# Optimization experiments

Hardware: AMD Instinct MI355X
Metric: run time of the kernel (lower is better)

Reference implementation:

```python
import jax, jax.numpy as jnp
import numpy as np

B, F = 1048576, 128


def setup_inputs() -> dict:
    key = jax.random.key(0)
    ks = jax.random.split(key, 16)
    def w(k, shape):
        return jax.random.normal(k, shape, dtype=jnp.float32) * 0.1
    x = jax.random.uniform(ks[0], (B, F), dtype=jnp.float32, minval=0.05, maxval=1.0)
    return {
        "x": x,
        "W_prod": w(ks[1], (F, 1)), "b_prod": w(ks[2], (1,)),
        "W_sum": w(ks[3], (F + 1, 1)), "b_sum": w(ks[4], (1,)),
        "w_dln": w(ks[5], (1, 1)), "W_ln": w(ks[6], (2, 1)),
        "w_dsin": w(ks[7], (1, 1)), "W_sin": w(ks[8], (2, 1)),
        "w_dcos": w(ks[9], (1, 1)), "W_cos": w(ks[10], (2, 1)),
        "w_de": w(ks[11], (1, 1)), "W_e": w(ks[12], (2, 1)),
        "w_dtanh": w(ks[13], (1, 1)), "W_tanh": w(ks[14], (2, 1)),
    }


def _stage(h, fn, w_drop, W):
    # h: [B,1]. Drop = Dense(1, relu, no bias) on fn(h); then Dense(2->1, no bias)
    d = jax.nn.relu(fn(h) * w_drop[0, 0])          # [B,1]
    return jnp.concatenate([d, h], axis=-1) @ W    # [B,1]


def reference(x, W_prod, b_prod, W_sum, b_sum,
              w_dln, W_ln, w_dsin, W_sin, w_dcos, W_cos,
              w_de, W_e, w_dtanh, W_tanh):
    # ProductBlock: exp(Dense(log(abs(x))))  -> product-of-powers via log-space
    x_prod = jnp.exp(jnp.log(jnp.abs(x)) @ W_prod + b_prod)          # [B,1]
    # SumBlock over [x, x_prod]
    x_sum = jnp.concatenate([x, x_prod], axis=-1) @ W_sum + b_sum    # [B,1]
    x_ln = _stage(x_sum, lambda t: jnp.log(jnp.abs(t)), w_dln, W_ln)
    x_sin = _stage(x_ln, jnp.sin, w_dsin, W_sin)
    x_cos = _stage(x_sin, jnp.cos, w_dcos, W_cos)
    x_e = _stage(x_cos, jnp.exp, w_de, W_e)
    x_tanh = _stage(x_e, jnp.tanh, w_dtanh, W_tanh)
    return x_tanh
```

## Files before the change

### kernel.cpp

```cpp
#include <hip/hip_runtime.h>


__global__ __launch_bounds__(256) void funcblock_kernel(
    const float* __restrict__ x,
    const float* __restrict__ W_prod, const float* __restrict__ b_prod,
    const float* __restrict__ W_sum,  const float* __restrict__ b_sum,
    const float* __restrict__ w_dln,  const float* __restrict__ W_ln,
    const float* __restrict__ w_dsin, const float* __restrict__ W_sin,
    const float* __restrict__ w_dcos, const float* __restrict__ W_cos,
    const float* __restrict__ w_de,   const float* __restrict__ W_e,
    const float* __restrict__ w_dtanh,const float* __restrict__ W_tanh,
    float* __restrict__ out, int B)
{
    __shared__ float pbuf[4][64];
    __shared__ float sbuf[4][64];

    const int tid   = threadIdx.x;
    const int hlane = tid & 31;
    const int half  = (tid >> 5) & 1;
    const int wid   = tid >> 6;
    const int lane  = tid & 63;

    const float4 wp = reinterpret_cast<const float4*>(W_prod)[hlane];
    const float4 ws = reinterpret_cast<const float4*>(W_sum)[hlane];
    const float ws128 = W_sum[128];
    const float bp2 = b_prod[0] * 1.44269504088896340736f;
    const float bs = b_sum[0];
    const float wdln  = w_dln[0],  wln0  = W_ln[0],  wln1  = W_ln[1];
    const float wdsin = w_dsin[0], wsin0 = W_sin[0], wsin1 = W_sin[1];
    const float wdcos = w_dcos[0], wcos0 = W_cos[0], wcos1 = W_cos[1];
    const float wde   = w_de[0],   we0   = W_e[0],   we1   = W_e[1];
    const float wdtanh= w_dtanh[0],wt0   = W_tanh[0],wt1   = W_tanh[1];

    const int rows_per_block = 256;
    for (int base = blockIdx.x * rows_per_block; base < B;
         base += gridDim.x * rows_per_block) {
        const int wbase = base + wid * 64;

        #pragma unroll 2
        for (int it = 0; it < 32; ++it) {
            const int row = wbase + half * 32 + it;
            float p = 0.0f, s = 0.0f;
            if (row < B) {
                const float4 xv =
                    reinterpret_cast<const float4*>(x + (size_t)row * 128)[hlane];
                p  = __log2f(__builtin_fabsf(xv.x)) * wp.x;
                p += __log2f(__builtin_fabsf(xv.y)) * wp.y;
                p += __log2f(__builtin_fabsf(xv.z)) * wp.z;
                p += __log2f(__builtin_fabsf(xv.w)) * wp.w;
                s  = xv.x * ws.x + xv.y * ws.y + xv.z * ws.z + xv.w * ws.w;
            }
            #pragma unroll
            for (int m = 16; m >= 1; m >>= 1) {
                p += __shfl_xor(p, m, 64);
                s += __shfl_xor(s, m, 64);
            }
            if (hlane == 0) {
                pbuf[wid][half * 32 + it] = p;
                sbuf[wid][half * 32 + it] = s;
            }
        }
        __syncthreads();

        const int row = wbase + lane;
        const float p = pbuf[wid][lane];
        const float s = sbuf[wid][lane];
        __syncthreads();

        const float x_prod = __builtin_amdgcn_exp2f(p + bp2);
        float h = s + x_prod * ws128 + bs;
        float d;
        d = fmaxf(logf(fabsf(h)) * wdln, 0.0f);  h = d * wln0  + h * wln1;
        d = fmaxf(sinf(h) * wdsin, 0.0f);        h = d * wsin0 + h * wsin1;
        d = fmaxf(cosf(h) * wdcos, 0.0f);        h = d * wcos0 + h * wcos1;
        d = fmaxf(expf(h) * wde,   0.0f);        h = d * we0   + h * we1;
        d = fmaxf(tanhf(h) * wdtanh, 0.0f);      h = d * wt0   + h * wt1;
        if (row < B) out[row] = h;
    }
}

extern "C" void kernel_launch(void* const* d_in, const int* in_sizes, int n_in,
                              void* d_out, int out_size, void* d_ws, size_t ws_size,
                              hipStream_t stream) {
    const float* x      = (const float*)d_in[0];
    const float* W_prod = (const float*)d_in[1];
    const float* b_prod = (const float*)d_in[2];
    const float* W_sum  = (const float*)d_in[3];
    const float* b_sum  = (const float*)d_in[4];
    const float* w_dln  = (const float*)d_in[5];
    const float* W_ln   = (const float*)d_in[6];
    const float* w_dsin = (const float*)d_in[7];
    const float* W_sin  = (const float*)d_in[8];
    const float* w_dcos = (const float*)d_in[9];
    const float* W_cos  = (const float*)d_in[10];
    const float* w_de   = (const float*)d_in[11];
    const float* W_e    = (const float*)d_in[12];
    const float* w_dtanh= (const float*)d_in[13];
    const float* W_tanh = (const float*)d_in[14];
    float* out = (float*)d_out;

    const int B = out_size;
    const int block = 256;
    const int grid  = 2048;

    hipLaunchKernelGGL(funcblock_kernel, dim3(grid), dim3(block), 0, stream,
                       x, W_prod, b_prod, W_sum, b_sum,
                       w_dln, W_ln, w_dsin, W_sin, w_dcos, W_cos,
                       w_de, W_e, w_dtanh, W_tanh, out, B);
}
```

Baseline: 105.0 us.

## Assign eight lanes per row with four float4 loads each to shorten shuffle reduction

Changes the work mapping so each row is handled by 8 lanes instead of 32, with each lane loading four float4 chunks strided by 8. The butterfly shuffle reduction drops from 5 steps to 3, and there are 8 loop iterations per wave instead of 32. This cuts the number of cross-lane shuffles and LDS writes per row and gives each lane more independent loads in flight. The cost is higher register use for the weight and x arrays.

```diff
diff --git a/kernel.cpp b/kernel.cpp
--- a/kernel.cpp
+++ b/kernel.cpp
@@ -15,14 +15,18 @@
     __shared__ float pbuf[4][64];
     __shared__ float sbuf[4][64];
 
-    const int tid   = threadIdx.x;
-    const int hlane = tid & 31;
-    const int half  = (tid >> 5) & 1;
-    const int wid   = tid >> 6;
-    const int lane  = tid & 63;
+    const int tid  = threadIdx.x;
+    const int lane = tid & 63;
+    const int wid  = tid >> 6;
+    const int u    = lane & 7;
+    const int g    = lane >> 3;
 
-    const float4 wp = reinterpret_cast<const float4*>(W_prod)[hlane];
-    const float4 ws = reinterpret_cast<const float4*>(W_sum)[hlane];
+    float4 wp[4], ws[4];
+    #pragma unroll
+    for (int j = 0; j < 4; ++j) {
+        wp[j] = reinterpret_cast<const float4*>(W_prod)[u + 8 * j];
+        ws[j] = reinterpret_cast<const float4*>(W_sum)[u + 8 * j];
+    }
     const float ws128 = W_sum[128];
     const float bp2 = b_prod[0] * 1.44269504088896340736f;
     const float bs = b_sum[0];
@@ -38,26 +42,33 @@
         const int wbase = base + wid * 64;
 
         #pragma unroll 2
-        for (int it = 0; it < 32; ++it) {
-            const int row = wbase + half * 32 + it;
+        for (int it = 0; it < 8; ++it) {
+            const int row = wbase + it * 8 + g;
             float p = 0.0f, s = 0.0f;
             if (row < B) {
-                const float4 xv =
-                    reinterpret_cast<const float4*>(x + (size_t)row * 128)[hlane];
-                p  = __log2f(__builtin_fabsf(xv.x)) * wp.x;
-                p += __log2f(__builtin_fabsf(xv.y)) * wp.y;
-                p += __log2f(__builtin_fabsf(xv.z)) * wp.z;
-                p += __log2f(__builtin_fabsf(xv.w)) * wp.w;
-                s  = xv.x * ws.x + xv.y * ws.y + xv.z * ws.z + xv.w * ws.w;
+                const float4* xr =
+                    reinterpret_cast<const float4*>(x + (size_t)row * 128);
+                float4 xv[4];
+                #pragma unroll
+                for (int j = 0; j < 4; ++j) xv[j] = xr[u + 8 * j];
+                #pragma unroll
+                for (int j = 0; j < 4; ++j) {
+                    p += __log2f(__builtin_fabsf(xv[j].x)) * wp[j].x;
+                    p += __log2f(__builtin_fabsf(xv[j].y)) * wp[j].y;
+                    p += __log2f(__builtin_fabsf(xv[j].z)) * wp[j].z;
+                    p += __log2f(__builtin_fabsf(xv[j].w)) * wp[j].w;
+                    s += xv[j].x * ws[j].x + xv[j].y * ws[j].y
+                       + xv[j].z * ws[j].z + xv[j].w * ws[j].w;
+                }
             }
             #pragma unroll
-            for (int m = 16; m >= 1; m >>= 1) {
+            for (int m = 4; m >= 1; m >>= 1) {
                 p += __shfl_xor(p, m, 64);
                 s += __shfl_xor(s, m, 64);
             }
-            if (hlane == 0) {
-                pbuf[wid][half * 32 + it] = p;
-                sbuf[wid][half * 32 + it] = s;
+            if (u == 0) {
+                pbuf[wid][it * 8 + g] = p;
+                sbuf[wid][it * 8 + g] = s;
             }
         }
         __syncthreads();
```

Measured after the change: 100.8 us. 4.0% less time.
